# Kernel optimization log

Hardware: AMD Instinct MI355X
Metric: run time of the kernel (lower is better)

The kernel has to match this reference:

```python
import jax, jax.numpy as jnp
import numpy as np

S, B, E, H = 2048, 1, 1024, 16
D = E // H                     # head_dim = 64
WINDOW = 1024                  # sliding_window_size
NEG_INF = jnp.float32(-1e30)


def setup_inputs() -> dict:
    key = jax.random.key(0)
    ks = jax.random.split(key, 8)
    w_scale = (2.0 / (E + E)) ** 0.5  # xavier_uniform-ish std
    inp = {
        "query": jax.random.normal(ks[0], (S, B, E), jnp.float32),
        "key": jax.random.normal(ks[1], (S, B, E), jnp.float32),
        "value": jax.random.normal(ks[2], (S, B, E), jnp.float32),
        "positions_bias": jax.random.normal(ks[3], (B * H, S, S), jnp.float32) * 0.1,
        "Wq": jax.random.normal(ks[4], (E, E), jnp.float32) * w_scale,
        "bq": jnp.zeros((E,), jnp.float32),
        "Wk": jax.random.normal(ks[5], (E, E), jnp.float32) * w_scale,
        "bk": jnp.zeros((E,), jnp.float32),
        "Wv": jax.random.normal(ks[6], (E, E), jnp.float32) * w_scale,
        "bv": jnp.zeros((E,), jnp.float32),
        "Wo": jax.random.normal(ks[7], (E, E), jnp.float32) * w_scale,
        "bo": jnp.zeros((E,), jnp.float32),
    }
    return inp


def _heads(x):
    # [S, B, E] -> [B, H, S, D]
    return x.reshape(S, B, H, D).transpose(1, 2, 0, 3)


def _stream(qh, kh, vh, bias, Wo, bo):
    scaling = D ** -0.5
    # NOTE: original pre-scales q by head_dim**-0.5 AND flex_attention applies
    # its default 1/sqrt(head_dim) scale -> effective q.k / head_dim.
    scores = jnp.einsum("bhqd,bhkd->bhqk", qh, kh) * scaling + bias
    qi = jnp.arange(S)[:, None]
    kj = jnp.arange(S)[None, :]
    mask = (qi >= kj) & (qi - kj <= WINDOW)  # causal + sliding window
    scores = jnp.where(mask, scores, NEG_INF)
    p = jax.nn.softmax(scores, axis=-1)
    o = jnp.einsum("bhqk,bhkd->bhqd", p, vh)
    o = o.transpose(2, 0, 1, 3).reshape(S, B, E)  # [S, B, E]
    return o @ Wo.T + bo


def reference(query, key, value, positions_bias, Wq, bq, Wk, bk, Wv, bv, Wo, bo):
    scaling = D ** -0.5
    kh = _heads(key @ Wk.T + bk)
    vh = _heads(value @ Wv.T + bv)
    # query passed as a single tensor -> c == q (non-tuple branch)
    ch = _heads((query @ Wq.T + bq) * scaling)
    bias = positions_bias.reshape(B, H, S, S)
    # content stream (attn_mask=None) and query stream (query_mask=None,
    # query_position_bias defaults to positions_bias) compute identical math
    # here since c == q; XLA will CSE the duplicate.
    c_out = _stream(ch, kh, vh, bias, Wo, bo)
    q_out = _stream(ch, kh, vh, bias, Wo, bo)
    return (c_out, q_out)
```

## Files before the change

kernel.cpp:

```cpp
#include <hip/hip_runtime.h>

typedef unsigned short u16;
typedef __bf16 bf16x8 __attribute__((ext_vector_type(8)));
typedef float f32x4 __attribute__((ext_vector_type(4)));

#define S_LEN 2048
#define EMB   1024
#define NHEAD 16
#define HDIM  64
#define WIN   1024

#define AS1 __attribute__((address_space(1)))
#define AS3 __attribute__((address_space(3)))

__device__ __forceinline__ u16 f2bf(float f) {
  unsigned u = __float_as_uint(f);
  u += 0x7FFFu + ((u >> 16) & 1u);
  return (u16)(u >> 16);
}

__global__ __launch_bounds__(256) void conv_kernel(
    const float* __restrict__ p0, const float* __restrict__ p1,
    const float* __restrict__ p2, const float* __restrict__ p3,
    const float* __restrict__ p4, const float* __restrict__ p5,
    const float* __restrict__ p6,
    u16* __restrict__ o0, u16* __restrict__ o1, u16* __restrict__ o2,
    u16* __restrict__ o3, u16* __restrict__ o4, u16* __restrict__ o5,
    u16* __restrict__ o6) {
  const float* src; u16* dst; int n;
  switch (blockIdx.y) {
    case 0: src = p0; dst = o0; n = S_LEN * EMB; break;
    case 1: src = p1; dst = o1; n = S_LEN * EMB; break;
    case 2: src = p2; dst = o2; n = S_LEN * EMB; break;
    case 3: src = p3; dst = o3; n = EMB * EMB; break;
    case 4: src = p4; dst = o4; n = EMB * EMB; break;
    case 5: src = p5; dst = o5; n = EMB * EMB; break;
    default: src = p6; dst = o6; n = EMB * EMB; break;
  }
  int i = (blockIdx.x * 256 + threadIdx.x) * 4;
  if (i >= n) return;
  float4 v = *reinterpret_cast<const float4*>(src + i);
  ushort4 r;
  r.x = f2bf(v.x); r.y = f2bf(v.y); r.z = f2bf(v.z); r.w = f2bf(v.w);
  *reinterpret_cast<ushort4*>(dst + i) = r;
}

__device__ __forceinline__ void gemm_128x64_core(
    const u16* __restrict__ A, const u16* __restrict__ W,
    const float* __restrict__ bias, float scale, int mode,
    u16* __restrict__ outB, float* __restrict__ outF0, float* __restrict__ outF1,
    int N, int K, int bm, int bn, u16* As, u16* Bs) {
  const int tid  = threadIdx.x;
  const int w    = tid >> 6;
  const int lane = tid & 63;
  const int wr = w >> 1, wc = w & 1;
  const int lr = lane & 15;
  const int ko = (lane >> 4) * 8;

  f32x4 acc[4][2];
#pragma unroll
  for (int i = 0; i < 4; ++i)
#pragma unroll
    for (int j = 0; j < 2; ++j) acc[i][j] = f32x4{0.f, 0.f, 0.f, 0.f};

  const int srow = lane >> 3;
  const int scol = (lane & 7) * 8;

  for (int k0 = 0; k0 < K; k0 += 64) {
    const u16* Ab = A + (size_t)bm * K + k0;
    const u16* Wb = W + (size_t)bn * K + k0;
#pragma unroll
    for (int c = 0; c < 4; ++c) {
      int s = w * 4 + c;
      __builtin_amdgcn_global_load_lds(
          (const AS1 void*)(Ab + (size_t)(s * 8 + srow) * K + scol),
          (AS3 void*)(As + s * 512), 16, 0, 0);
    }
#pragma unroll
    for (int c = 0; c < 2; ++c) {
      int s = w * 2 + c;
      __builtin_amdgcn_global_load_lds(
          (const AS1 void*)(Wb + (size_t)(s * 8 + srow) * K + scol),
          (AS3 void*)(Bs + s * 512), 16, 0, 0);
    }
    __syncthreads();
#pragma unroll
    for (int kk = 0; kk < 2; ++kk) {
      bf16x8 af[4], bfr[2];
#pragma unroll
      for (int mi = 0; mi < 4; ++mi)
        af[mi] = *reinterpret_cast<const bf16x8*>(&As[(wr * 64 + mi * 16 + lr) * 64 + kk * 32 + ko]);
#pragma unroll
      for (int ni = 0; ni < 2; ++ni)
        bfr[ni] = *reinterpret_cast<const bf16x8*>(&Bs[(wc * 32 + ni * 16 + lr) * 64 + kk * 32 + ko]);
#pragma unroll
      for (int mi = 0; mi < 4; ++mi)
#pragma unroll
        for (int ni = 0; ni < 2; ++ni)
          acc[mi][ni] = __builtin_amdgcn_mfma_f32_16x16x32_bf16(af[mi], bfr[ni], acc[mi][ni], 0, 0, 0);
    }
    __syncthreads();
  }

  const int cr = (lane >> 4) * 4;
  const int cc = lane & 15;

  if (mode == 2) {
#pragma unroll
    for (int mi = 0; mi < 4; ++mi) {
#pragma unroll
      for (int ni = 0; ni < 2; ++ni) {
        int dd0 = wc * 32 + ni * 16 + cc;
        float bv = bias[bn + dd0];
#pragma unroll
        for (int r = 0; r < 4; ++r) {
          int rp = wr * 64 + mi * 16 + cr + r;
          As[dd0 * 128 + (rp ^ ((dd0 & 7) * 8))] = f2bf((acc[mi][ni][r] + bv) * scale);
        }
      }
    }
    __syncthreads();
    const int h = bn >> 6;
    u16* Vb = outB + (size_t)h * (HDIM * S_LEN);
    const int dd = tid >> 4;
    const int ch = tid & 15;
#pragma unroll
    for (int i = 0; i < 4; ++i) {
      int d = dd + i * 16;
      const u16* src = &As[d * 128 + ((ch ^ (d & 7)) * 8)];
      u16* dst = Vb + (size_t)d * S_LEN + bm + ch * 8;
      *reinterpret_cast<ushort4*>(dst)     = *reinterpret_cast<const ushort4*>(src);
      *reinterpret_cast<ushort4*>(dst + 4) = *reinterpret_cast<const ushort4*>(src + 4);
    }
    return;
  }

#pragma unroll
  for (int mi = 0; mi < 4; ++mi) {
#pragma unroll
    for (int ni = 0; ni < 2; ++ni) {
      int col = bn + wc * 32 + ni * 16 + cc;
      float bv = bias[col];
#pragma unroll
      for (int r = 0; r < 4; ++r) {
        int row = bm + wr * 64 + mi * 16 + cr + r;
        float val = (acc[mi][ni][r] + bv) * scale;
        if (mode == 1) {
          size_t idx = (size_t)(col >> 6) * (S_LEN * HDIM) + (size_t)row * HDIM + (col & 63);
          outB[idx] = f2bf(val);
        } else {
          outF0[(size_t)row * N + col] = val;
          outF1[(size_t)row * N + col] = val;
        }
      }
    }
  }
}

__device__ __forceinline__ void supertile_decode(int bx, int& bm, int& bn) {
  int sb = bx >> 4, inner = bx & 15;
  bm = ((sb >> 2) * 4 + (inner >> 2)) * 128;
  bn = ((sb & 3) * 4 + (inner & 3)) * 64;
}

__global__ __launch_bounds__(256, 4) void proj_gemm(
    const u16* __restrict__ Abase, const u16* __restrict__ Wbase,
    const float* __restrict__ b0, const float* __restrict__ b1,
    const float* __restrict__ b2, u16* __restrict__ Qp,
    u16* __restrict__ Kp, u16* __restrict__ Vt) {
  __shared__ u16 As[128 * 64];
  __shared__ u16 Bs[64 * 64];
  const int z = blockIdx.z;
  const u16* A = Abase + (size_t)z * (S_LEN * EMB);
  const u16* W = Wbase + (size_t)z * (EMB * EMB);
  const float* bias = (z == 0) ? b0 : (z == 1 ? b1 : b2);
  u16* O = (z == 0) ? Qp : (z == 1 ? Kp : Vt);
  float scale = (z == 0) ? (1.0f / 64.0f) : 1.0f;
  int bm, bn;
  supertile_decode(blockIdx.x, bm, bn);
  gemm_128x64_core(A, W, bias, scale, (z == 2) ? 2 : 1, O, nullptr, nullptr,
                   EMB, EMB, bm, bn, As, Bs);
}

__global__ __launch_bounds__(256, 4) void out_gemm(
    const u16* __restrict__ A, const u16* __restrict__ W,
    const float* __restrict__ bias, float* __restrict__ out0,
    float* __restrict__ out1) {
  __shared__ u16 As[128 * 64];
  __shared__ u16 Bs[64 * 64];
  int bm, bn;
  supertile_decode(blockIdx.x, bm, bn);
  gemm_128x64_core(A, W, bias, 1.0f, 0, nullptr, out0, out1,
                   EMB, EMB, bm, bn, As, Bs);
}

__global__ __launch_bounds__(128, 2) void attn_kernel(
    const u16* __restrict__ Qp, const u16* __restrict__ Kp,
    const u16* __restrict__ Vt, const float* __restrict__ pbias,
    u16* __restrict__ Ob) {
  __shared__ u16 KV[2][2][64 * 64];
  __shared__ u16 Pb[2][16 * 64];

  const int tid  = threadIdx.x;
  const int w    = tid >> 6;
  const int lane = tid & 63;

  const int d   = blockIdx.x + 64 * blockIdx.y;
  const int xcd = d & 7;
  const int s   = d >> 3;
  const int h   = xcd * 2 + (s >> 6);
  const int q0  = (63 - (s & 63)) * 32;

  const int ql = lane & 15;
  const int g  = lane >> 4;
  const int qw = q0 + w * 16;
  const int qg = qw + ql;
  const int qw_hi = qw + 15;

  const u16* Kh  = Kp + (size_t)h * (S_LEN * HDIM);
  const u16* Vth = Vt + (size_t)h * (HDIM * S_LEN);

  const u16* Qrow = Qp + (size_t)h * (S_LEN * HDIM) + (size_t)qg * HDIM;
  bf16x8 qf0 = *reinterpret_cast<const bf16x8*>(&Qrow[g * 8]);
  bf16x8 qf1 = *reinterpret_cast<const bf16x8*>(&Qrow[32 + g * 8]);

  f32x4 o[4];
#pragma unroll
  for (int i = 0; i < 4; ++i) o[i] = f32x4{0.f, 0.f, 0.f, 0.f};
  float m = -1e30f, l = 0.f;

  const float* brow = pbias + (size_t)h * S_LEN * S_LEN + (size_t)qg * S_LEN + 4 * g;

  int kv_lo = q0 - WIN; if (kv_lo < 0) kv_lo = 0; kv_lo &= ~63;
  const int ntiles = ((q0 + 31 - kv_lo) >> 6) + 1;
  const int kv_last = kv_lo + (ntiles - 1) * 64;

  const int swz = (ql & 7) << 4;
  char* Prow = (char*)&Pb[w][0] + ql * 128;

  auto STAGE = [&](int buf, int kv0) {
    u16* Kd = &KV[buf][0][(w * 32) * 64];
    u16* Vd = &KV[buf][1][(w * 32) * 64];
#pragma unroll
    for (int n = 0; n < 4; ++n) {
      int r  = w * 32 + n * 8 + (lane >> 3);
      int cp = (lane & 7) ^ (r & 7);
      __builtin_amdgcn_global_load_lds(
          (const AS1 void*)(Kh + (size_t)(kv0 + r) * HDIM + cp * 8),
          (AS3 void*)(Kd + n * 512), 16, 0, 0);
      __builtin_amdgcn_global_load_lds(
          (const AS1 void*)(Vth + (size_t)r * S_LEN + kv0 + cp * 8),
          (AS3 void*)(Vd + n * 512), 16, 0, 0);
    }
  };

  STAGE(0, kv_lo);
  float4 nb[4], cb[4];
#pragma unroll
  for (int kt = 0; kt < 4; ++kt)
    nb[kt] = *reinterpret_cast<const float4*>(&brow[kv_lo + kt * 16]);
  int cur = 0;

  for (int t = 0; t < ntiles; ++t) {
    const int kv0 = kv_lo + t * 64;
    __syncthreads();
#pragma unroll
    for (int kt = 0; kt < 4; ++kt) cb[kt] = nb[kt];

    if (t + 1 < ntiles) STAGE(cur ^ 1, kv0 + 64);
    const int nxt = (kv0 + 64 <= kv_last) ? kv0 + 64 : kv0;
#pragma unroll
    for (int kt = 0; kt < 4; ++kt)
      nb[kt] = *reinterpret_cast<const float4*>(&brow[nxt + kt * 16]);

    const bool active = (kv0 <= qw_hi) && (kv0 + 63 >= qw - WIN);
    if (active) {
      const char* Kl = (const char*)&KV[cur][0][0];
      const char* Vl = (const char*)&KV[cur][1][0];

      f32x4 s4[4];
#pragma unroll
      for (int kt = 0; kt < 4; ++kt) {
        bf16x8 ka = *reinterpret_cast<const bf16x8*>(Kl + (kt * 16 + ql) * 128 + ((g * 16) ^ swz));
        bf16x8 kb = *reinterpret_cast<const bf16x8*>(Kl + (kt * 16 + ql) * 128 + ((64 + g * 16) ^ swz));
        f32x4 acc = f32x4{0.f, 0.f, 0.f, 0.f};
        acc = __builtin_amdgcn_mfma_f32_16x16x32_bf16(ka, qf0, acc, 0, 0, 0);
        acc = __builtin_amdgcn_mfma_f32_16x16x32_bf16(kb, qf1, acc, 0, 0, 0);
        s4[kt] = acc;
      }

      const bool full = (kv0 + 63 <= qw) && (qw_hi - kv0 <= WIN);
      float lmax = -INFINITY;
#pragma unroll
      for (int kt = 0; kt < 4; ++kt) {
        float bvr[4] = {cb[kt].x, cb[kt].y, cb[kt].z, cb[kt].w};
#pragma unroll
        for (int r = 0; r < 4; ++r) {
          int k = kv0 + kt * 16 + 4 * g + r;
          float xv = s4[kt][r] + bvr[r];
          if (!full) {
            bool ok = (k <= qg) && ((qg - k) <= WIN);
            xv = ok ? xv : -INFINITY;
          }
          s4[kt][r] = xv;
          lmax = fmaxf(lmax, xv);
        }
      }
      lmax = fmaxf(lmax, __shfl_xor(lmax, 16));
      lmax = fmaxf(lmax, __shfl_xor(lmax, 32));
      float mn = fmaxf(m, lmax);
      float corr = __expf(m - mn);
      m = mn;
      float ls = 0.f;
#pragma unroll
      for (int kt = 0; kt < 4; ++kt)
#pragma unroll
        for (int r = 0; r < 4; ++r) {
          float e = __expf(s4[kt][r] - mn);
          s4[kt][r] = e;
          ls += e;
        }
      ls += __shfl_xor(ls, 16);
      ls += __shfl_xor(ls, 32);
      l = l * corr + ls;
#pragma unroll
      for (int dt = 0; dt < 4; ++dt) {
        f32x4 tt = o[dt];
#pragma unroll
        for (int r = 0; r < 4; ++r) tt[r] *= corr;
        o[dt] = tt;
      }

#pragma unroll
      for (int kt = 0; kt < 4; ++kt) {
        ushort4 pw;
        pw.x = f2bf(s4[kt][0]); pw.y = f2bf(s4[kt][1]);
        pw.z = f2bf(s4[kt][2]); pw.w = f2bf(s4[kt][3]);
        *reinterpret_cast<ushort4*>(Prow + ((kt * 32 + g * 8) ^ swz)) = pw;
      }
#pragma unroll
      for (int kb = 0; kb < 2; ++kb) {
        bf16x8 pf = *reinterpret_cast<const bf16x8*>(Prow + ((kb * 64 + g * 16) ^ swz));
#pragma unroll
        for (int dt = 0; dt < 4; ++dt) {
          bf16x8 vf = *reinterpret_cast<const bf16x8*>(Vl + (dt * 16 + ql) * 128 + ((kb * 64 + g * 16) ^ swz));
          o[dt] = __builtin_amdgcn_mfma_f32_16x16x32_bf16(vf, pf, o[dt], 0, 0, 0);
        }
      }
    }
    cur ^= 1;
  }

  float inv = (l > 0.f) ? 1.f / l : 0.f;
  u16* op = &Ob[(size_t)qg * EMB + h * HDIM];
#pragma unroll
  for (int dt = 0; dt < 4; ++dt) {
    ushort4 outv;
#pragma unroll
    for (int r = 0; r < 4; ++r) ((u16*)&outv)[r] = f2bf(o[dt][r] * inv);
    *reinterpret_cast<ushort4*>(op + dt * 16 + 4 * g) = outv;
  }
}

extern "C" void kernel_launch(void* const* d_in, const int* in_sizes, int n_in,
                              void* d_out, int out_size, void* d_ws, size_t ws_size,
                              hipStream_t stream) {
  (void)in_sizes; (void)n_in; (void)out_size; (void)ws_size;
  const float* q  = (const float*)d_in[0];
  const float* k  = (const float*)d_in[1];
  const float* v  = (const float*)d_in[2];
  const float* pb = (const float*)d_in[3];
  const float* Wq = (const float*)d_in[4];
  const float* bq = (const float*)d_in[5];
  const float* Wk = (const float*)d_in[6];
  const float* bk = (const float*)d_in[7];
  const float* Wv = (const float*)d_in[8];
  const float* bv = (const float*)d_in[9];
  const float* Wo = (const float*)d_in[10];
  const float* bo = (const float*)d_in[11];
  float* out = (float*)d_out;

  const size_t SE = (size_t)S_LEN * EMB;
  const size_t EE = (size_t)EMB * EMB;
  u16* ws  = (u16*)d_ws;
  u16* qb  = ws;
  u16* kb  = qb + SE;
  u16* vb  = kb + SE;
  u16* wqb = vb + SE;
  u16* wkb = wqb + EE;
  u16* wvb = wkb + EE;
  u16* wob = wvb + EE;
  u16* Qp  = wob + EE;
  u16* Kp  = Qp + SE;
  u16* Vt  = Kp + SE;
  u16* Ob  = Vt + SE;

  conv_kernel<<<dim3(2048, 7), 256, 0, stream>>>(q, k, v, Wq, Wk, Wv, Wo,
                                                 qb, kb, vb, wqb, wkb, wvb, wob);
  proj_gemm<<<dim3(256, 1, 3), 256, 0, stream>>>(qb, wqb, bq, bk, bv, Qp, Kp, Vt);
  attn_kernel<<<dim3(64, 16), 128, 0, stream>>>(Qp, Kp, Vt, pb, Ob);
  out_gemm<<<dim3(256), 256, 0, stream>>>(Ob, wob, bo, out, out + SE);
}
```

Baseline: 95.78 us.

## Restructure attention to single-wave blocks with 32-wide KV tiles and vmcnt pipelining

The attention kernel goes from 128-thread blocks (two waves, 32 queries, 64-wide KV tiles) to 64-thread single-wave blocks with 16 queries and 32-wide KV tiles. This doubles the grid. The __syncthreads is replaced by an explicit s_waitcnt vmcnt with a sched barrier, so the next tile's global-to-LDS loads overlap compute without block-level synchronisation. The aim is finer-grained work that tracks the causal/window mask more tightly, plus lower sync cost and higher occupancy. In exchange, K/V loads are no longer shared by two waves, which doubles K/V traffic per query. Correctness now depends on the hand-counted vmcnt value and a single-wave LDS ordering.

```diff
diff --git a/kernel.cpp b/kernel.cpp
--- a/kernel.cpp
+++ b/kernel.cpp
@@ -194,28 +194,26 @@
                    EMB, EMB, bm, bn, As, Bs);
 }
 
-__global__ __launch_bounds__(128, 2) void attn_kernel(
+__global__ __launch_bounds__(64, 2) void attn_kernel(
     const u16* __restrict__ Qp, const u16* __restrict__ Kp,
     const u16* __restrict__ Vt, const float* __restrict__ pbias,
     u16* __restrict__ Ob) {
-  __shared__ u16 KV[2][2][64 * 64];
-  __shared__ u16 Pb[2][16 * 64];
-
-  const int tid  = threadIdx.x;
-  const int w    = tid >> 6;
-  const int lane = tid & 63;
-
-  const int d   = blockIdx.x + 64 * blockIdx.y;
+  __shared__ u16 Ks[2][32 * 64];
+  __shared__ u16 Vs[2][64 * 32];
+  __shared__ u16 Ps[16 * 32];
+
+  const int lane = threadIdx.x;
+
+  const int d   = blockIdx.x + 128 * blockIdx.y;
   const int xcd = d & 7;
   const int s   = d >> 3;
-  const int h   = xcd * 2 + (s >> 6);
-  const int q0  = (63 - (s & 63)) * 32;
+  const int h   = xcd * 2 + (s >> 7);
+  const int q0  = (127 - (s & 127)) * 16;
 
   const int ql = lane & 15;
   const int g  = lane >> 4;
-  const int qw = q0 + w * 16;
-  const int qg = qw + ql;
-  const int qw_hi = qw + 15;
+  const int qg = q0 + ql;
+  const int q_hi = q0 + 15;
 
   const u16* Kh  = Kp + (size_t)h * (S_LEN * HDIM);
   const u16* Vth = Vt + (size_t)h * (HDIM * S_LEN);
@@ -231,122 +229,118 @@
 
   const float* brow = pbias + (size_t)h * S_LEN * S_LEN + (size_t)qg * S_LEN + 4 * g;
 
-  int kv_lo = q0 - WIN; if (kv_lo < 0) kv_lo = 0; kv_lo &= ~63;
-  const int ntiles = ((q0 + 31 - kv_lo) >> 6) + 1;
-  const int kv_last = kv_lo + (ntiles - 1) * 64;
-
-  const int swz = (ql & 7) << 4;
-  char* Prow = (char*)&Pb[w][0] + ql * 128;
+  int kv_lo = q0 - WIN; if (kv_lo < 0) kv_lo = 0; kv_lo &= ~31;
+  const int ntiles = ((q0 + 15 - kv_lo) >> 5) + 1;
+
+  const int swzK = (ql & 7) << 4;
+  const int swzP = (ql & 3) << 4;
+  char* Prow = (char*)Ps + ql * 64;
 
   auto STAGE = [&](int buf, int kv0) {
-    u16* Kd = &KV[buf][0][(w * 32) * 64];
-    u16* Vd = &KV[buf][1][(w * 32) * 64];
 #pragma unroll
     for (int n = 0; n < 4; ++n) {
-      int r  = w * 32 + n * 8 + (lane >> 3);
+      int r  = n * 8 + (lane >> 3);
       int cp = (lane & 7) ^ (r & 7);
       __builtin_amdgcn_global_load_lds(
           (const AS1 void*)(Kh + (size_t)(kv0 + r) * HDIM + cp * 8),
-          (AS3 void*)(Kd + n * 512), 16, 0, 0);
+          (AS3 void*)(&Ks[buf][n * 512]), 16, 0, 0);
+    }
+#pragma unroll
+    for (int n = 0; n < 4; ++n) {
+      int r  = n * 16 + (lane >> 2);
+      int cv = (lane & 3) ^ (r & 3);
       __builtin_amdgcn_global_load_lds(
-          (const AS1 void*)(Vth + (size_t)r * S_LEN + kv0 + cp * 8),
-          (AS3 void*)(Vd + n * 512), 16, 0, 0);
+          (const AS1 void*)(Vth + (size_t)r * S_LEN + kv0 + cv * 8),
+          (AS3 void*)(&Vs[buf][n * 512]), 16, 0, 0);
     }
   };
 
   STAGE(0, kv_lo);
-  float4 nb[4], cb[4];
-#pragma unroll
-  for (int kt = 0; kt < 4; ++kt)
-    nb[kt] = *reinterpret_cast<const float4*>(&brow[kv_lo + kt * 16]);
+  float4 nb0 = *reinterpret_cast<const float4*>(&brow[kv_lo]);
+  float4 nb1 = *reinterpret_cast<const float4*>(&brow[kv_lo + 16]);
   int cur = 0;
 
   for (int t = 0; t < ntiles; ++t) {
-    const int kv0 = kv_lo + t * 64;
-    __syncthreads();
-#pragma unroll
-    for (int kt = 0; kt < 4; ++kt) cb[kt] = nb[kt];
-
-    if (t + 1 < ntiles) STAGE(cur ^ 1, kv0 + 64);
-    const int nxt = (kv0 + 64 <= kv_last) ? kv0 + 64 : kv0;
-#pragma unroll
-    for (int kt = 0; kt < 4; ++kt)
-      nb[kt] = *reinterpret_cast<const float4*>(&brow[nxt + kt * 16]);
-
-    const bool active = (kv0 <= qw_hi) && (kv0 + 63 >= qw - WIN);
-    if (active) {
-      const char* Kl = (const char*)&KV[cur][0][0];
-      const char* Vl = (const char*)&KV[cur][1][0];
-
-      f32x4 s4[4];
-#pragma unroll
-      for (int kt = 0; kt < 4; ++kt) {
-        bf16x8 ka = *reinterpret_cast<const bf16x8*>(Kl + (kt * 16 + ql) * 128 + ((g * 16) ^ swz));
-        bf16x8 kb = *reinterpret_cast<const bf16x8*>(Kl + (kt * 16 + ql) * 128 + ((64 + g * 16) ^ swz));
-        f32x4 acc = f32x4{0.f, 0.f, 0.f, 0.f};
-        acc = __builtin_amdgcn_mfma_f32_16x16x32_bf16(ka, qf0, acc, 0, 0, 0);
-        acc = __builtin_amdgcn_mfma_f32_16x16x32_bf16(kb, qf1, acc, 0, 0, 0);
-        s4[kt] = acc;
+    const int kv0 = kv_lo + t * 32;
+    const int nxt = (t + 1 < ntiles) ? kv0 + 32 : kv_lo;
+
+    STAGE(cur ^ 1, nxt);
+    float4 cb0 = nb0, cb1 = nb1;
+    nb0 = *reinterpret_cast<const float4*>(&brow[nxt]);
+    nb1 = *reinterpret_cast<const float4*>(&brow[nxt + 16]);
+
+    asm volatile("s_waitcnt vmcnt(10)" ::: "memory");
+    __builtin_amdgcn_sched_barrier(0);
+
+    const char* Kl = (const char*)&Ks[cur][0];
+    const char* Vl = (const char*)&Vs[cur][0];
+
+    f32x4 s4[2];
+#pragma unroll
+    for (int kt = 0; kt < 2; ++kt) {
+      bf16x8 ka  = *reinterpret_cast<const bf16x8*>(Kl + (kt * 16 + ql) * 128 + ((g * 16) ^ swzK));
+      bf16x8 kb2 = *reinterpret_cast<const bf16x8*>(Kl + (kt * 16 + ql) * 128 + ((64 + g * 16) ^ swzK));
+      f32x4 acc = f32x4{0.f, 0.f, 0.f, 0.f};
+      acc = __builtin_amdgcn_mfma_f32_16x16x32_bf16(ka,  qf0, acc, 0, 0, 0);
+      acc = __builtin_amdgcn_mfma_f32_16x16x32_bf16(kb2, qf1, acc, 0, 0, 0);
+      s4[kt] = acc;
+    }
+
+    const bool full = (kv0 + 31 <= q0) && (q_hi - kv0 <= WIN);
+    float bv[2][4] = {{cb0.x, cb0.y, cb0.z, cb0.w},
+                      {cb1.x, cb1.y, cb1.z, cb1.w}};
+    float lmax = -INFINITY;
+#pragma unroll
+    for (int kt = 0; kt < 2; ++kt)
+#pragma unroll
+      for (int r = 0; r < 4; ++r) {
+        int k = kv0 + kt * 16 + 4 * g + r;
+        float xv = s4[kt][r] + bv[kt][r];
+        if (!full) {
+          bool ok = (k <= qg) && ((qg - k) <= WIN);
+          xv = ok ? xv : -INFINITY;
+        }
+        s4[kt][r] = xv;
+        lmax = fmaxf(lmax, xv);
       }
-
-      const bool full = (kv0 + 63 <= qw) && (qw_hi - kv0 <= WIN);
-      float lmax = -INFINITY;
-#pragma unroll
-      for (int kt = 0; kt < 4; ++kt) {
-        float bvr[4] = {cb[kt].x, cb[kt].y, cb[kt].z, cb[kt].w};
-#pragma unroll
-        for (int r = 0; r < 4; ++r) {
-          int k = kv0 + kt * 16 + 4 * g + r;
-          float xv = s4[kt][r] + bvr[r];
-          if (!full) {
-            bool ok = (k <= qg) && ((qg - k) <= WIN);
-            xv = ok ? xv : -INFINITY;
-          }
-          s4[kt][r] = xv;
-          lmax = fmaxf(lmax, xv);
-        }
+    lmax = fmaxf(lmax, __shfl_xor(lmax, 16));
+    lmax = fmaxf(lmax, __shfl_xor(lmax, 32));
+    float mn = fmaxf(m, lmax);
+    float corr = __expf(m - mn);
+    m = mn;
+    float ls = 0.f;
+#pragma unroll
+    for (int kt = 0; kt < 2; ++kt)
+#pragma unroll
+      for (int r = 0; r < 4; ++r) {
+        float e = __expf(s4[kt][r] - mn);
+        s4[kt][r] = e;
+        ls += e;
       }
-      lmax = fmaxf(lmax, __shfl_xor(lmax, 16));
-      lmax = fmaxf(lmax, __shfl_xor(lmax, 32));
-      float mn = fmaxf(m, lmax);
-      float corr = __expf(m - mn);
-      m = mn;
-      float ls = 0.f;
-#pragma unroll
-      for (int kt = 0; kt < 4; ++kt)
-#pragma unroll
-        for (int r = 0; r < 4; ++r) {
-          float e = __expf(s4[kt][r] - mn);
-          s4[kt][r] = e;
-          ls += e;
-        }
-      ls += __shfl_xor(ls, 16);
-      ls += __shfl_xor(ls, 32);
-      l = l * corr + ls;
-#pragma unroll
-      for (int dt = 0; dt < 4; ++dt) {
-        f32x4 tt = o[dt];
-#pragma unroll
-        for (int r = 0; r < 4; ++r) tt[r] *= corr;
-        o[dt] = tt;
-      }
-
-#pragma unroll
-      for (int kt = 0; kt < 4; ++kt) {
-        ushort4 pw;
-        pw.x = f2bf(s4[kt][0]); pw.y = f2bf(s4[kt][1]);
-        pw.z = f2bf(s4[kt][2]); pw.w = f2bf(s4[kt][3]);
-        *reinterpret_cast<ushort4*>(Prow + ((kt * 32 + g * 8) ^ swz)) = pw;
-      }
-#pragma unroll
-      for (int kb = 0; kb < 2; ++kb) {
-        bf16x8 pf = *reinterpret_cast<const bf16x8*>(Prow + ((kb * 64 + g * 16) ^ swz));
-#pragma unroll
-        for (int dt = 0; dt < 4; ++dt) {
-          bf16x8 vf = *reinterpret_cast<const bf16x8*>(Vl + (dt * 16 + ql) * 128 + ((kb * 64 + g * 16) ^ swz));
-          o[dt] = __builtin_amdgcn_mfma_f32_16x16x32_bf16(vf, pf, o[dt], 0, 0, 0);
-        }
-      }
+    ls += __shfl_xor(ls, 16);
+    ls += __shfl_xor(ls, 32);
+    l = l * corr + ls;
+#pragma unroll
+    for (int dt = 0; dt < 4; ++dt) {
+      f32x4 tt = o[dt];
+#pragma unroll
+      for (int r = 0; r < 4; ++r) tt[r] *= corr;
+      o[dt] = tt;
+    }
+
+#pragma unroll
+    for (int kt = 0; kt < 2; ++kt) {
+      ushort4 pw;
+      pw.x = f2bf(s4[kt][0]); pw.y = f2bf(s4[kt][1]);
+      pw.z = f2bf(s4[kt][2]); pw.w = f2bf(s4[kt][3]);
+      *reinterpret_cast<ushort4*>(Prow + ((kt * 32 + g * 8) ^ swzP)) = pw;
+    }
+    bf16x8 pf = *reinterpret_cast<const bf16x8*>(Prow + ((g * 16) ^ swzP));
+    const int vchunk = (g ^ (ql & 3)) * 16;
+#pragma unroll
+    for (int dt = 0; dt < 4; ++dt) {
+      bf16x8 vf = *reinterpret_cast<const bf16x8*>(Vl + (dt * 16 + ql) * 64 + vchunk);
+      o[dt] = __builtin_amdgcn_mfma_f32_16x16x32_bf16(vf, pf, o[dt], 0, 0, 0);
     }
     cur ^= 1;
   }
@@ -398,6 +392,6 @@
   conv_kernel<<<dim3(2048, 7), 256, 0, stream>>>(q, k, v, Wq, Wk, Wv, Wo,
                                                  qb, kb, vb, wqb, wkb, wvb, wob);
   proj_gemm<<<dim3(256, 1, 3), 256, 0, stream>>>(qb, wqb, bq, bk, bv, Qp, Kp, Vt);
-  attn_kernel<<<dim3(64, 16), 128, 0, stream>>>(Qp, Kp, Vt, pb, Ob);
+  attn_kernel<<<dim3(128, 16), 64, 0, stream>>>(Qp, Kp, Vt, pb, Ob);
   out_gemm<<<dim3(256), 256, 0, stream>>>(Ob, wob, bo, out, out + SE);
 }
```

After: 106.7 us. 1.11x slower.
